# Kernel optimization log

Hardware: AMD Instinct MI355X
Metric: run time of the kernel (lower is better)

Reference implementation:

```python
import jax, jax.numpy as jnp
import numpy as np


def setup_inputs() -> dict:
    key = jax.random.key(0)
    ks = jax.random.split(key, 4)
    B, N, K, C = 1, 8192, 32, 21
    S = jax.random.randint(ks[0], (B, N), 0, C, dtype=jnp.int64)
    h = jax.random.normal(ks[1], (B, N, C), dtype=jnp.float32)
    J = jax.random.normal(ks[2], (B, N, K, C, C), dtype=jnp.float32)
    edge_idx = jax.random.randint(ks[3], (B, N, K), 0, N, dtype=jnp.int64)
    mask_i = jnp.ones((B, N), dtype=jnp.float32)
    mask_ij = jnp.ones((B, N, K), dtype=jnp.float32)
    return {"S": S, "h": h, "J": J, "edge_idx": edge_idx,
            "mask_i": mask_i, "mask_ij": mask_ij}


def reference(S, h, J, edge_idx, mask_i, mask_ij):
    """Potts energy: U (B,), U_i (B,N,C). Same math as _compute_potts_energy_reduced."""
    B, N, K = edge_idx.shape
    C = h.shape[-1]
    h = h * mask_i[..., None]
    J = J * mask_ij[..., None, None]
    # collect neighbor states: S_j[b,i,k] = S[b, edge_idx[b,i,k]]  -> (B,N,K)
    S_j = jnp.take_along_axis(S, edge_idx.reshape(B, N * K), axis=1).reshape(B, N, K)
    # gather coupling column per neighbor state: J_ij[b,i,k,c] = J[b,i,k,c,S_j[b,i,k]]
    idx = jnp.broadcast_to(S_j[:, :, :, None, None], (B, N, K, C, 1))
    J_ij = jnp.take_along_axis(J, idx, axis=-1)[..., 0]          # (B,N,K,C)
    J_i = J_ij.sum(axis=2)                                        # (B,N,C)
    U_i = h + J_i                                                 # (B,N,C)
    U_sel = jnp.take_along_axis(U_i, S[..., None], axis=-1)[..., 0]  # (B,N)
    J_sel = jnp.take_along_axis(J_i, S[..., None], axis=-1)[..., 0]  # (B,N)
    U = (U_sel - 0.5 * J_sel).sum(axis=1)                         # (B,)
    return U, U_i
```

## Files before the change

### kernel.cpp

```cpp
#include <hip/hip_runtime.h>
#include <hip/hip_bf16.h>


#define KK 32
#define CC 21
#define BLOCK_ELEMS (KK * CC * CC)
#define BLOCK_VEC4  (BLOCK_ELEMS / 4)

__global__ __launch_bounds__(256) void potts_kernel(
    const int* __restrict__ S,
    const float* __restrict__ h,
    const float* __restrict__ J,
    const int* __restrict__ edge_idx,
    const float* __restrict__ mask_i,
    const float* __restrict__ mask_ij,
    float* __restrict__ out)
{
    const int i   = blockIdx.x;
    const int tid = threadIdx.x;

    __shared__ int   s_j[KK];
    __shared__ float m_ij[KK];
    __shared__ float acc[CC];
    __shared__ float ui_s[CC];

    if (tid < KK) {
        int e = edge_idx[i * KK + tid];
        s_j[tid]  = S[e];
        m_ij[tid] = mask_ij[i * KK + tid];
    }
    if (tid < CC) acc[tid] = 0.0f;
    __syncthreads();

    const float4* __restrict__ Jb =
        (const float4*)(J + (size_t)i * BLOCK_ELEMS);

    for (int q = tid; q < BLOCK_VEC4; q += 256) {
        float4 v = Jb[q];
        const float* vf = (const float*)&v;
        int e0 = q * 4;
#pragma unroll
        for (int j = 0; j < 4; ++j) {
            int e  = e0 + j;
            int k  = e / (CC * CC);
            int c2 = e % CC;
            if (c2 == s_j[k]) {
                int c = (e - k * (CC * CC)) / CC;
                atomicAdd(&acc[c], vf[j] * m_ij[k]);
            }
        }
    }
    __syncthreads();

    if (tid < CC) {
        float ui = h[i * CC + tid] * mask_i[i] + acc[tid];
        out[1 + i * CC + tid] = ui;
        ui_s[tid] = ui;
    }
    __syncthreads();

    if (tid == 0) {
        int s = S[i];
        float u = ui_s[s] - 0.5f * acc[s];
        atomicAdd(out, u);
    }
}

extern "C" void kernel_launch(void* const* d_in, const int* in_sizes, int n_in,
                              void* d_out, int out_size, void* d_ws, size_t ws_size,
                              hipStream_t stream) {
    const int*   S        = (const int*)d_in[0];
    const float* h        = (const float*)d_in[1];
    const float* J        = (const float*)d_in[2];
    const int*   edge_idx = (const int*)d_in[3];
    const float* mask_i   = (const float*)d_in[4];
    const float* mask_ij  = (const float*)d_in[5];
    float* out = (float*)d_out;

    const int N = in_sizes[0];

    hipMemsetAsync(out, 0, sizeof(float), stream);

    potts_kernel<<<N, 256, 0, stream>>>(S, h, J, edge_idx, mask_i, mask_ij, out);
}
```

Before: 644.6 us.

## Gather only the needed coupling entries instead of streaming the full J block

```diff
diff --git a/kernel.cpp b/kernel.cpp
--- a/kernel.cpp
+++ b/kernel.cpp
@@ -4,8 +4,7 @@
 
 #define KK 32
 #define CC 21
-#define BLOCK_ELEMS (KK * CC * CC)
-#define BLOCK_VEC4  (BLOCK_ELEMS / 4)
+#define PAIRS (KK * CC)
 
 __global__ __launch_bounds__(256) void potts_kernel(
     const int* __restrict__ S,
@@ -32,23 +31,26 @@
     if (tid < CC) acc[tid] = 0.0f;
     __syncthreads();
 
-    const float4* __restrict__ Jb =
-        (const float4*)(J + (size_t)i * BLOCK_ELEMS);
+    const float* __restrict__ Jb = J + (size_t)i * (KK * CC * CC);
 
-    for (int q = tid; q < BLOCK_VEC4; q += 256) {
-        float4 v = Jb[q];
-        const float* vf = (const float*)&v;
-        int e0 = q * 4;
+    float vals[3];
+    int   cs[3];
 #pragma unroll
-        for (int j = 0; j < 4; ++j) {
-            int e  = e0 + j;
-            int k  = e / (CC * CC);
-            int c2 = e % CC;
-            if (c2 == s_j[k]) {
-                int c = (e - k * (CC * CC)) / CC;
-                atomicAdd(&acc[c], vf[j] * m_ij[k]);
-            }
+    for (int j = 0; j < 3; ++j) {
+        int idx = tid + j * 256;
+        if (idx < PAIRS) {
+            int k = idx / CC;
+            int c = idx - k * CC;
+            cs[j]   = c;
+            vals[j] = Jb[k * (CC * CC) + c * CC + s_j[k]] * m_ij[k];
+        } else {
+            cs[j]   = -1;
+            vals[j] = 0.0f;
         }
+    }
+#pragma unroll
+    for (int j = 0; j < 3; ++j) {
+        if (cs[j] >= 0) atomicAdd(&acc[cs[j]], vals[j]);
     }
     __syncthreads();
 
```

Result: faster. 630.0 us (-2.3%).
